# Kernel optimization log

Measured on AMD Instinct MI355X. Metric: run time of the kernel, lower is better.

Reference implementation:

```python
import jax, jax.numpy as jnp
import numpy as np

N, E = 50000, 800000
IN, HID, OUT, L = 512, 64, 40, 16
ALPHA, LAMBDA = 0.1, 0.5


def setup_inputs() -> dict:
    key = jax.random.key(0)
    ks = jax.random.split(key, 8)
    features = jax.random.normal(ks[0], (N, IN), jnp.float32)
    src = jax.random.randint(ks[1], (E,), 0, N)
    dst = jax.random.randint(ks[2], (E,), 0, N)
    # fcs[0]: Linear(IN, HID); fcs[1]: Linear(HID, OUT)
    W_in = jax.random.normal(ks[3], (IN, HID), jnp.float32) / np.sqrt(IN)
    b_in = jnp.zeros((HID,), jnp.float32)
    W_out = jax.random.normal(ks[4], (HID, OUT), jnp.float32) / np.sqrt(HID)
    b_out = jnp.zeros((OUT,), jnp.float32)
    # per-layer GCN2Conv weights (project_initial_features=False -> weight1 & weight2) + bias
    W1 = jax.random.normal(ks[5], (L, HID, HID), jnp.float32) / np.sqrt(HID)
    W2 = jax.random.normal(ks[6], (L, HID, HID), jnp.float32) / np.sqrt(HID)
    b = jnp.zeros((L, HID), jnp.float32)
    return dict(features=features, W_in=W_in, b_in=b_in, W1=W1, W2=W2, b=b,
                W_out=W_out, b_out=b_out, src=src, dst=dst)


def reference(features, W_in, b_in, W1, W2, b, W_out, b_out, src, dst):
    ones = jnp.ones((E,), jnp.float32)
    deg_out = jax.ops.segment_sum(ones, src, num_segments=N)
    deg_in = jax.ops.segment_sum(ones, dst, num_segments=N)
    norm_src = jnp.maximum(deg_out, 1.0) ** -0.5  # [N]
    norm_dst = jnp.maximum(deg_in, 1.0) ** -0.5   # [N]
    betas = jnp.log(LAMBDA / jnp.arange(1, L + 1, dtype=jnp.float32) + 1.0)

    # inference: dropout is identity
    h0 = jax.nn.relu(features @ W_in + b_in)  # [N, HID]

    def layer(h, params):
        w1, w2, bias, beta = params
        # symmetric-normalized sparse propagation: D^-1/2 A D^-1/2 h
        hs = h * norm_src[:, None]
        agg = jax.ops.segment_sum(hs[src], dst, num_segments=N) * norm_dst[:, None]
        f = (1.0 - ALPHA) * agg   # smoothed part
        f0 = ALPHA * h0           # initial residual
        rst = (1.0 - beta) * f + beta * (f @ w1)
        rst = rst + (1.0 - beta) * f0 + beta * (f0 @ w2)
        rst = rst + bias
        return jax.nn.relu(rst), None

    h, _ = jax.lax.scan(layer, h0, (W1, W2, b, betas))
    logits = h @ W_out + b_out  # [N, OUT]
    return jax.nn.log_softmax(logits, axis=1)
```

## Files before the change

### kernel.cpp

```cpp
#include <hip/hip_runtime.h>
#include <math.h>

#define NN 50000
#define NE 800000
#define INF 512
#define HID 64
#define OUTF 40
#define NL 16

#define NBLK 256
#define EPB 3125
#define NBUK 196
#define SLEN (NBUK * NBLK)

#define TN 32
#define FP 72

using short8 = __attribute__((ext_vector_type(8))) short;
using f32x4v = __attribute__((ext_vector_type(4))) float;

__device__ __forceinline__ unsigned int f2bf(float f) {
    unsigned int u = __float_as_uint(f);
    return (u + 0x7fffu + ((u >> 16) & 1u)) >> 16;
}
__device__ __forceinline__ float bflo(unsigned int w) { return __uint_as_float(w << 16); }
__device__ __forceinline__ float bfhi(unsigned int w) { return __uint_as_float(w & 0xffff0000u); }
__device__ __forceinline__ float bfs(unsigned short u) { return __uint_as_float(((unsigned)u) << 16); }


__global__ __launch_bounds__(256) void k_cnt(const int* __restrict__ src, const int* __restrict__ dst,
                                             int* __restrict__ cnt2) {
    __shared__ int hD[NBUK];
    __shared__ int hS[NBUK];
    int t = threadIdx.x;
    int blk = blockIdx.x;
    if (t < NBUK) { hD[t] = 0; hS[t] = 0; }
    __syncthreads();
    int s0 = blk * EPB;
    for (int i = t; i < EPB; i += 256) {
        int e = s0 + i;
        atomicAdd(&hD[dst[e] >> 8], 1);
        atomicAdd(&hS[src[e] >> 8], 1);
    }
    __syncthreads();
    if (t < NBUK) {
        cnt2[t * NBLK + blk] = hD[t];
        cnt2[SLEN + t * NBLK + blk] = hS[t];
    }
}

__global__ __launch_bounds__(256) void gscanA(const int* __restrict__ in, int* __restrict__ incl,
                                              int* __restrict__ bsum, int len) {
    __shared__ int lds[256];
    int i = blockIdx.x * 256 + threadIdx.x;
    int v = (i < len) ? in[i] : 0;
    lds[threadIdx.x] = v;
    __syncthreads();
    for (int off = 1; off < 256; off <<= 1) {
        int t = (threadIdx.x >= off) ? lds[threadIdx.x - off] : 0;
        __syncthreads();
        lds[threadIdx.x] += t;
        __syncthreads();
    }
    if (i < len) incl[i] = lds[threadIdx.x];
    if (threadIdx.x == 255) bsum[blockIdx.x] = lds[255];
}

__global__ __launch_bounds__(512) void gscanB(int* __restrict__ bsum, int nb) {
    __shared__ int lds[512];
    int v = (threadIdx.x < nb) ? bsum[threadIdx.x] : 0;
    lds[threadIdx.x] = v;
    __syncthreads();
    for (int off = 1; off < 512; off <<= 1) {
        int t = (threadIdx.x >= off) ? lds[threadIdx.x - off] : 0;
        __syncthreads();
        lds[threadIdx.x] += t;
        __syncthreads();
    }
    if (threadIdx.x < nb) bsum[threadIdx.x] = lds[threadIdx.x] - v;
}

__global__ __launch_bounds__(256) void gscanC(const int* __restrict__ incl, const int* __restrict__ in,
                                              const int* __restrict__ bsum, int* __restrict__ off, int len) {
    int i = blockIdx.x * 256 + threadIdx.x;
    if (i < len) off[i] = incl[i] - in[i] + bsum[i >> 8] - ((i >= SLEN) ? NE : 0);
}

__global__ __launch_bounds__(256) void k_scat(const int* __restrict__ src, const int* __restrict__ dst,
                                              const int* __restrict__ offD, const int* __restrict__ offS,
                                              uint2* __restrict__ edst, int* __restrict__ esrc) {
    __shared__ int cD[NBUK];
    __shared__ int cS[NBUK];
    int t = threadIdx.x;
    int blk = blockIdx.x;
    if (t < NBUK) { cD[t] = 0; cS[t] = 0; }
    __syncthreads();
    int s0 = blk * EPB;
    for (int i = t; i < EPB; i += 256) {
        int e = s0 + i;
        int d = dst[e];
        int s = src[e];
        int bD = d >> 8;
        int r = atomicAdd(&cD[bD], 1);
        uint2 v;
        v.x = (unsigned)d;
        v.y = (unsigned)s;
        edst[offD[bD * NBLK + blk] + r] = v;
        int bS = s >> 8;
        int r2 = atomicAdd(&cS[bS], 1);
        esrc[offS[bS * NBLK + blk] + r2] = s;
    }
}

__global__ __launch_bounds__(256) void k_build(const uint2* __restrict__ edst, const int* __restrict__ esrc,
                                               const int* __restrict__ offD, const int* __restrict__ offS,
                                               float* __restrict__ nd, int* __restrict__ row_start,
                                               int* __restrict__ col, float* __restrict__ ns) {
    __shared__ int cnt[256];
    __shared__ int ex[256];
    __shared__ int cur[256];
    int t = threadIdx.x;
    if (blockIdx.x < NBUK) {
        int b = blockIdx.x;
        int base = offD[b * NBLK];
        int end = (b < NBUK - 1) ? offD[(b + 1) * NBLK] : NE;
        cnt[t] = 0;
        __syncthreads();
        for (int p = base + t; p < end; p += 256) {
            uint2 ed = edst[p];
            atomicAdd(&cnt[ed.x & 255], 1);
        }
        __syncthreads();
        int v = cnt[t];
        ex[t] = v;
        __syncthreads();
        for (int off = 1; off < 256; off <<= 1) {
            int tv = (t >= off) ? ex[t - off] : 0;
            __syncthreads();
            ex[t] += tv;
            __syncthreads();
        }
        int excl = ex[t] - v;
        cur[t] = excl;
        int node = b * 256 + t;
        if (node < NN) {
            nd[node] = 1.0f / sqrtf((float)max(v, 1));
            row_start[node] = base + excl;
        }
        __syncthreads();
        for (int p = base + t; p < end; p += 256) {
            uint2 ed = edst[p];
            int r = atomicAdd(&cur[ed.x & 255], 1);
            col[base + r] = (int)ed.y;
        }
    } else {
        int b = blockIdx.x - NBUK;
        int base = offS[b * NBLK];
        int end = (b < NBUK - 1) ? offS[(b + 1) * NBLK] : NE;
        cnt[t] = 0;
        __syncthreads();
        for (int p = base + t; p < end; p += 256) {
            atomicAdd(&cnt[esrc[p] & 255], 1);
        }
        __syncthreads();
        int node = b * 256 + t;
        if (node < NN) ns[node] = 1.0f / sqrtf((float)max(cnt[t], 1));
    }
}

__global__ __launch_bounds__(256) void k_wpp(const float* __restrict__ W1, const float* __restrict__ W2,
                                             const float* __restrict__ Win,
                                             unsigned short* __restrict__ wc, unsigned short* __restrict__ wf) {
    int o = blockIdx.x * 256 + threadIdx.x;
    const int NWC = NL * 4 * 4 * 64 * 8;
    if (o < NWC) {
        int j = o & 7;
        int ln = (o >> 3) & 63;
        int c = (o >> 9) & 3;
        int s = (o >> 11) & 3;
        int l = o >> 13;
        int colg = c * 16 + (ln & 15);
        int k = (s & 1) * 32 + ((ln >> 4) << 3) + j;
        float beta = logf(0.5f / (float)(l + 1) + 1.0f);
        const float* W = (s < 2) ? W1 : W2;
        wc[o] = (unsigned short)f2bf(beta * W[((size_t)l * 64 + k) * 64 + colg]);
    } else if (o < NWC + 16 * 4 * 64 * 8) {
        int o2 = o - NWC;
        int jj = o2 & 7;
        int l = (o2 >> 3) & 63;
        int c = (o2 >> 9) & 3;
        int s = o2 >> 11;
        int colg = c * 16 + (l & 15);
        int k = s * 32 + ((l >> 4) << 3) + jj;
        wf[o2] = (unsigned short)f2bf(Win[k * HID + colg]);
    }
}

__global__ __launch_bounds__(256) void k_gemm0(const float* __restrict__ feat, const unsigned short* __restrict__ wf,
                                               float* __restrict__ p0, float* __restrict__ p1) {
    __shared__ unsigned int fS[2048];
    int tid = threadIdx.x;
    int lane = tid & 63;
    int wv = tid >> 6;
    int bx = blockIdx.x;
    int w = bx >> 1;
    int kh = bx & 1;
    int nb = w * 64;
    f32x4v acc[4];
#pragma unroll
    for (int c = 0; c < 4; c++) acc[c] = {0.0f, 0.0f, 0.0f, 0.0f};

    int k0 = kh * 256;
    for (int kc = k0; kc < k0 + 256; kc += 64) {
        if (kc != k0) __syncthreads();
        float4 t[4];
#pragma unroll
        for (int j = 0; j < 4; j++) {
            int i = tid + j * 256;
            int nl = i >> 4;
            int k4 = i & 15;
            int n = min(nb + nl, NN - 1);
            t[j] = *(const float4*)(feat + (size_t)n * INF + kc + k4 * 4);
        }
#pragma unroll
        for (int j = 0; j < 4; j++) {
            int i = tid + j * 256;
            int nl = i >> 4;
            int kl = (i & 15) * 4;
            int s = kl >> 5;
            int kk = kl & 31;
            int lslot = (nl & 15) | ((kk >> 3) << 4);
            int dstu = (((s * 4 + (nl >> 4)) * 64 + lslot) << 2) + ((kk & 4) >> 1);
            fS[dstu] = f2bf(t[j].x) | (f2bf(t[j].y) << 16);
            fS[dstu + 1] = f2bf(t[j].z) | (f2bf(t[j].w) << 16);
        }
        __syncthreads();
#pragma unroll
        for (int s = 0; s < 2; ++s) {
            int sg = (kc + s * 32) >> 5;
            short8 af = *(const short8*)&fS[((s * 4 + wv) * 64 + lane) << 2];
            short8 bf[4];
#pragma unroll
            for (int c = 0; c < 4; ++c)
                bf[c] = *(const short8*)(wf + ((size_t)(sg * 4 + c) * 64 + lane) * 8);
#pragma unroll
            for (int c = 0; c < 4; ++c)
                acc[c] = __builtin_amdgcn_mfma_f32_16x16x32_bf16(af, bf[c], acc[c], 0, 0, 0);
        }
    }
    float* p = kh ? p1 : p0;
    int nodeb = nb + (wv << 4) + ((lane >> 4) << 2);
    int colb = lane & 15;
#pragma unroll
    for (int r = 0; r < 4; ++r) {
        int node = nodeb + r;
        if (node < NN) {
            float* pp = p + (size_t)node * HID + colb;
#pragma unroll
            for (int c = 0; c < 4; ++c) pp[c * 16] = acc[c][r];
        }
    }
}

__global__ __launch_bounds__(256) void k_gfin(const float* __restrict__ p0, const float* __restrict__ p1,
                                              const float* __restrict__ bin, const float* __restrict__ ns,
                                              unsigned int* __restrict__ hs, unsigned int* __restrict__ f0b) {
    int i = blockIdx.x * 256 + threadIdx.x;
    if (i >= NN * 16) return;
    int node = i >> 4;
    int q = i & 15;
    float4 a = ((const float4*)p0)[i];
    float4 b = ((const float4*)p1)[i];
    float4 bi = ((const float4*)bin)[q];
    float nsv = ns[node];
    float q0 = fmaxf(a.x + b.x + bi.x, 0.0f);
    float q1 = fmaxf(a.y + b.y + bi.y, 0.0f);
    float q2 = fmaxf(a.z + b.z + bi.z, 0.0f);
    float q3 = fmaxf(a.w + b.w + bi.w, 0.0f);
    uint2 pk;
    pk.x = f2bf(q0 * nsv) | (f2bf(q1 * nsv) << 16);
    pk.y = f2bf(q2 * nsv) | (f2bf(q3 * nsv) << 16);
    *(uint2*)(hs + (size_t)node * 32 + q * 2) = pk;
    uint2 pf;
    pf.x = f2bf(q0 * 0.1f) | (f2bf(q1 * 0.1f) << 16);
    pf.y = f2bf(q2 * 0.1f) | (f2bf(q3 * 0.1f) << 16);
    *(uint2*)(f0b + (size_t)node * 32 + q * 2) = pf;
}

__global__ __launch_bounds__(256) void k_layer(const unsigned int* __restrict__ hs_in, const int* __restrict__ col,
                                               const int* __restrict__ row_start,
                                               const float* __restrict__ nd, const unsigned int* __restrict__ f0b,
                                               const unsigned short* __restrict__ wc, const float* __restrict__ bias,
                                               const float* __restrict__ ns, float omb,
                                               float* __restrict__ h, unsigned int* __restrict__ hs_out, int write_h) {
    __shared__ unsigned short fS[TN * FP];
    __shared__ unsigned short f0S[TN * FP];
    __shared__ unsigned short oS[TN * FP];
    __shared__ float nsS[TN];
    int tid = threadIdx.x;
    int lane = tid & 63;
    int wv = tid >> 6;
    int nb = blockIdx.x * TN;
    int g = lane >> 4;
    int ql = lane & 15;
    int half = ql >> 3;
    int qb = ql & 7;

    {
        int nl = tid >> 3, sg = tid & 7;
        int n = min(nb + nl, NN - 1);
        uint4 v = *(const uint4*)(f0b + (size_t)n * 32 + sg * 4);
        *(uint4*)&f0S[nl * FP + sg * 8] = v;
    }
    if (tid < TN) nsS[tid] = ns[min(nb + tid, NN - 1)];

    int nlP[2], baseP[2], degP[2], idxP[2];
    float ndP[2];
#pragma unroll
    for (int p = 0; p < 2; ++p) {
        int nl = p * 16 + wv * 4 + g;
        int n = min(nb + nl, NN - 1);
        nlP[p] = nl;
        int base = row_start[n];
        int nxt = (n < NN - 1) ? row_start[n + 1] : NE;
        baseP[p] = base;
        degP[p] = nxt - base;
        ndP[p] = nd[n];
    }
#pragma unroll
    for (int p = 0; p < 2; ++p) {
        idxP[p] = (ql < min(16, degP[p])) ? col[baseP[p] + ql] : 0;
    }

#pragma unroll
    for (int pass = 0; pass < 2; ++pass) {
        int base = baseP[pass];
        int deg = degP[pass];
        int idxv = idxP[pass];
        float a0 = 0.f, a1 = 0.f, a2 = 0.f, a3 = 0.f, a4 = 0.f, a5 = 0.f, a6 = 0.f, a7 = 0.f;
        for (int done = 0; done < deg; done += 16) {
            int cnt = min(16, deg - done);
            int nxt = done + 16;
            int idxn = 0;
            if (nxt < deg && ql < deg - nxt) idxn = col[base + nxt + ql];
            uint4 pv[4];
#pragma unroll
            for (int e = 0; e < 4; ++e) {
                int ec = 2 * e + half;
                int s = __shfl(idxv, (g << 4) | ec, 64);
                uint4 v = {0u, 0u, 0u, 0u};
                if (ec < cnt) v = *(const uint4*)(hs_in + (size_t)s * 32 + qb * 4);
                pv[e] = v;
            }
#pragma unroll
            for (int e = 0; e < 4; ++e) {
                a0 += bflo(pv[e].x); a1 += bfhi(pv[e].x);
                a2 += bflo(pv[e].y); a3 += bfhi(pv[e].y);
                a4 += bflo(pv[e].z); a5 += bfhi(pv[e].z);
                a6 += bflo(pv[e].w); a7 += bfhi(pv[e].w);
            }
#pragma unroll
            for (int e = 0; e < 4; ++e) {
                int ec = 8 + 2 * e + half;
                int s = __shfl(idxv, (g << 4) | ec, 64);
                uint4 v = {0u, 0u, 0u, 0u};
                if (ec < cnt) v = *(const uint4*)(hs_in + (size_t)s * 32 + qb * 4);
                pv[e] = v;
            }
#pragma unroll
            for (int e = 0; e < 4; ++e) {
                a0 += bflo(pv[e].x); a1 += bfhi(pv[e].x);
                a2 += bflo(pv[e].y); a3 += bfhi(pv[e].y);
                a4 += bflo(pv[e].z); a5 += bfhi(pv[e].z);
                a6 += bflo(pv[e].w); a7 += bfhi(pv[e].w);
            }
            idxv = idxn;
        }
        a0 += __shfl_xor(a0, 8, 64);
        a1 += __shfl_xor(a1, 8, 64);
        a2 += __shfl_xor(a2, 8, 64);
        a3 += __shfl_xor(a3, 8, 64);
        a4 += __shfl_xor(a4, 8, 64);
        a5 += __shfl_xor(a5, 8, 64);
        a6 += __shfl_xor(a6, 8, 64);
        a7 += __shfl_xor(a7, 8, 64);
        float sc = 0.9f * ndP[pass];
        int nl = nlP[pass];
        if (half == 0) {
            uint4 w;
            w.x = f2bf(a0 * sc) | (f2bf(a1 * sc) << 16);
            w.y = f2bf(a2 * sc) | (f2bf(a3 * sc) << 16);
            w.z = f2bf(a4 * sc) | (f2bf(a5 * sc) << 16);
            w.w = f2bf(a6 * sc) | (f2bf(a7 * sc) << 16);
            *(uint4*)&fS[nl * FP + qb * 8] = w;
        }
    }
    __syncthreads();

    int hi = lane >> 4;
    int lo = lane & 15;
    f32x4v acc0 = {0.0f, 0.0f, 0.0f, 0.0f};
    f32x4v acc1 = {0.0f, 0.0f, 0.0f, 0.0f};
#pragma unroll
    for (int s = 0; s < 4; ++s) {
        short8 bf = *(const short8*)(wc + ((size_t)(s * 4 + wv) * 64 + lane) * 8);
        const unsigned short* ab = (s < 2) ? fS : f0S;
        int ko = (s & 1) * 32;
        short8 a0 = *(const short8*)&ab[(0 * 16 + lo) * FP + ko + hi * 8];
        short8 a1 = *(const short8*)&ab[(1 * 16 + lo) * FP + ko + hi * 8];
        acc0 = __builtin_amdgcn_mfma_f32_16x16x32_bf16(a0, bf, acc0, 0, 0, 0);
        acc1 = __builtin_amdgcn_mfma_f32_16x16x32_bf16(a1, bf, acc1, 0, 0, 0);
    }

    int colg = wv * 16 + lo;
    float bv = bias[colg];
#pragma unroll
    for (int m = 0; m < 2; ++m) {
        f32x4v a = m ? acc1 : acc0;
#pragma unroll
        for (int r = 0; r < 4; ++r) {
            int rowl = m * 16 + hi * 4 + r;
            float fv = bfs(fS[rowl * FP + colg]);
            float f0v = bfs(f0S[rowl * FP + colg]);
            float q = fmaxf(a[r] + omb * (fv + f0v) + bv, 0.0f);
            oS[rowl * FP + colg] = (unsigned short)f2bf(q * nsS[rowl]);
            if (write_h) {
                int node = nb + rowl;
                if (node < NN) h[(size_t)node * HID + colg] = q;
            }
        }
    }
    __syncthreads();

    {
        int nl = tid >> 3, sg = tid & 7;
        int node = nb + nl;
        if (node < NN) {
            uint4 v = *(const uint4*)&oS[nl * FP + sg * 8];
            *(uint4*)(hs_out + (size_t)node * 32 + sg * 4) = v;
        }
    }
}

__global__ __launch_bounds__(256) void k_out(const float* __restrict__ h, const float* __restrict__ Wout,
                                             const float* __restrict__ bout, float* __restrict__ out) {
    __shared__ float red_mx[4][64];
    __shared__ float red_s[4][64];
    int tid = threadIdx.x;
    int lane = tid & 63;
    int wv = tid >> 6;
    int half = wv & 1;
    int grp = wv >> 1;
    int node = blockIdx.x * 128 + grp * 64 + lane;
    int nodec = min(node, NN - 1);
    float acc[20];
#pragma unroll
    for (int c = 0; c < 20; c++) acc[c] = 0.0f;
    const float4* hr = (const float4*)(h + (size_t)nodec * HID);
    const float* wb = Wout + half * 20;
    for (int kk = 0; kk < HID / 4; ++kk) {
        float4 a = hr[kk];
        float av[4] = {a.x, a.y, a.z, a.w};
#pragma unroll
        for (int j = 0; j < 4; j++) {
            const float* wr = wb + (size_t)(kk * 4 + j) * OUTF;
#pragma unroll
            for (int c = 0; c < 20; c++) acc[c] += av[j] * wr[c];
        }
    }
    const float* bp = bout + half * 20;
#pragma unroll
    for (int c = 0; c < 20; c++) acc[c] += bp[c];
    float mx = acc[0];
#pragma unroll
    for (int c = 1; c < 20; c++) mx = fmaxf(mx, acc[c]);
    red_mx[wv][lane] = mx;
    __syncthreads();
    float gmx = fmaxf(mx, red_mx[wv ^ 1][lane]);
    float s = 0.0f;
#pragma unroll
    for (int c = 0; c < 20; c++) s += expf(acc[c] - gmx);
    red_s[wv][lane] = s;
    __syncthreads();
    float lse = logf(s + red_s[wv ^ 1][lane]) + gmx;
    if (node < NN) {
        float4* op = (float4*)(out + (size_t)node * OUTF + half * 20);
#pragma unroll
        for (int q = 0; q < 5; q++) {
            float4 v;
            v.x = acc[q * 4 + 0] - lse;
            v.y = acc[q * 4 + 1] - lse;
            v.z = acc[q * 4 + 2] - lse;
            v.w = acc[q * 4 + 3] - lse;
            op[q] = v;
        }
    }
}

extern "C" void kernel_launch(void* const* d_in, const int* in_sizes, int n_in,
                              void* d_out, int out_size, void* d_ws, size_t ws_size,
                              hipStream_t stream) {
    const float* feat = (const float*)d_in[0];
    const float* Win  = (const float*)d_in[1];
    const float* bin  = (const float*)d_in[2];
    const float* W1   = (const float*)d_in[3];
    const float* W2   = (const float*)d_in[4];
    const float* bvec = (const float*)d_in[5];
    const float* Wout = (const float*)d_in[6];
    const float* bout = (const float*)d_in[7];
    const int*   src  = (const int*)d_in[8];
    const int*   dst  = (const int*)d_in[9];
    float* out = (float*)d_out;

    char* ws = (char*)d_ws;
    size_t off = 0;
    auto take = [&](size_t bytes) {
        void* p = ws + off;
        off += (bytes + 255) & ~(size_t)255;
        return p;
    };
    int* bsum      = (int*)take(512 * 4);
    int* row_start = (int*)take(NN * 4);
    int* col       = (int*)take(NE * 4);
    float* nsrc    = (float*)take(NN * 4);
    float* ndst    = (float*)take(NN * 4);
    int* cnt2      = (int*)take(2 * SLEN * 4);
    int* off2      = (int*)take(2 * SLEN * 4);
    int* sincl     = (int*)take(2 * SLEN * 4);
    unsigned short* wcat  = (unsigned short*)take((size_t)NL * 4 * 4 * 64 * 8 * 2);
    unsigned short* wfrag = (unsigned short*)take((size_t)INF * HID * 2);
    unsigned int* f0b = (unsigned int*)take((size_t)NN * HID * 2);
    float* hbuf    = (float*)take((size_t)NN * HID * 4);
    float* part1   = (float*)take((size_t)NN * HID * 4);
    unsigned int* hsA = (unsigned int*)take((size_t)NN * HID * 2);
    unsigned int* hsB = (unsigned int*)take((size_t)NN * HID * 2);

    uint2* edst = (uint2*)hbuf;
    int* esrc   = (int*)part1;
    int* offD = off2;
    int* offS = off2 + SLEN;

    const int NB_W = (NN + 63) / 64;
    const int NB_L = (NN + TN - 1) / TN;
    const int NB_O = (NN + 127) / 128;
    const int NB_S2 = 2 * SLEN / 256;

    k_cnt<<<NBLK, 256, 0, stream>>>(src, dst, cnt2);
    gscanA<<<NB_S2, 256, 0, stream>>>(cnt2, sincl, bsum, 2 * SLEN);
    gscanB<<<1, 512, 0, stream>>>(bsum, NB_S2);
    gscanC<<<NB_S2, 256, 0, stream>>>(sincl, cnt2, bsum, off2, 2 * SLEN);
    k_scat<<<NBLK, 256, 0, stream>>>(src, dst, offD, offS, edst, esrc);
    k_build<<<2 * NBUK, 256, 0, stream>>>(edst, esrc, offD, offS, ndst, row_start, col, nsrc);

    k_wpp<<<(NL * 4 * 4 * 64 * 8 + INF * HID + 255) / 256, 256, 0, stream>>>(W1, W2, Win, wcat, wfrag);
    k_gemm0<<<2 * NB_W, 256, 0, stream>>>(feat, wfrag, hbuf, part1);
    k_gfin<<<(NN * 16 + 255) / 256, 256, 0, stream>>>(hbuf, part1, bin, nsrc, hsA, f0b);

    for (int l = 0; l < NL; ++l) {
        const unsigned int* hin = (l & 1) ? hsB : hsA;
        unsigned int* hout = (l & 1) ? hsA : hsB;
        float beta = logf(0.5f / (float)(l + 1) + 1.0f);
        float omb = 1.0f - beta;
        k_layer<<<NB_L, 256, 0, stream>>>(hin, col, row_start, ndst, f0b,
                                          wcat + (size_t)l * 4 * 4 * 64 * 8, bvec + l * HID,
                                          nsrc, omb, hbuf, hout, (l == NL - 1) ? 1 : 0);
    }
    k_out<<<NB_O, 256, 0, stream>>>(hbuf, Wout, bout, out);
}
```

Measured before the change: 557.5 us.

## Balance layer aggregation across edges with packed dst ids and LDS atomic accumulation

```diff
diff --git a/kernel.cpp b/kernel.cpp
--- a/kernel.cpp
+++ b/kernel.cpp
@@ -15,6 +15,7 @@
 
 #define TN 32
 #define FP 72
+#define TNP 33
 
 using short8 = __attribute__((ext_vector_type(8))) short;
 using f32x4v = __attribute__((ext_vector_type(4))) float;
@@ -115,7 +116,7 @@
 __global__ __launch_bounds__(256) void k_build(const uint2* __restrict__ edst, const int* __restrict__ esrc,
                                                const int* __restrict__ offD, const int* __restrict__ offS,
                                                float* __restrict__ nd, int* __restrict__ row_start,
-                                               int* __restrict__ col, float* __restrict__ ns) {
+                                               int* __restrict__ epk, float* __restrict__ ns) {
     __shared__ int cnt[256];
     __shared__ int ex[256];
     __shared__ int cur[256];
@@ -151,7 +152,7 @@
         for (int p = base + t; p < end; p += 256) {
             uint2 ed = edst[p];
             int r = atomicAdd(&cur[ed.x & 255], 1);
-            col[base + r] = (int)ed.y;
+            epk[base + r] = (int)((ed.y << 5) | (ed.x & 31u));
         }
     } else {
         int b = blockIdx.x - NBUK;
@@ -287,16 +288,18 @@
     *(uint2*)(f0b + (size_t)node * 32 + q * 2) = pf;
 }
 
-__global__ __launch_bounds__(256) void k_layer(const unsigned int* __restrict__ hs_in, const int* __restrict__ col,
+__global__ __launch_bounds__(256) void k_layer(const unsigned int* __restrict__ hs_in, const int* __restrict__ epk,
                                                const int* __restrict__ row_start,
                                                const float* __restrict__ nd, const unsigned int* __restrict__ f0b,
                                                const unsigned short* __restrict__ wc, const float* __restrict__ bias,
                                                const float* __restrict__ ns, float omb,
                                                float* __restrict__ h, unsigned int* __restrict__ hs_out, int write_h) {
+    __shared__ float fT32[HID * TNP];
     __shared__ unsigned short fS[TN * FP];
     __shared__ unsigned short f0S[TN * FP];
     __shared__ unsigned short oS[TN * FP];
     __shared__ float nsS[TN];
+    __shared__ float ndS[TN];
     int tid = threadIdx.x;
     int lane = tid & 63;
     int wv = tid >> 6;
@@ -306,94 +309,98 @@
     int half = ql >> 3;
     int qb = ql & 7;
 
+    for (int i = tid; i < HID * TNP; i += 256) fT32[i] = 0.0f;
     {
         int nl = tid >> 3, sg = tid & 7;
         int n = min(nb + nl, NN - 1);
         uint4 v = *(const uint4*)(f0b + (size_t)n * 32 + sg * 4);
         *(uint4*)&f0S[nl * FP + sg * 8] = v;
     }
-    if (tid < TN) nsS[tid] = ns[min(nb + tid, NN - 1)];
-
-    int nlP[2], baseP[2], degP[2], idxP[2];
-    float ndP[2];
-#pragma unroll
-    for (int p = 0; p < 2; ++p) {
-        int nl = p * 16 + wv * 4 + g;
-        int n = min(nb + nl, NN - 1);
-        nlP[p] = nl;
-        int base = row_start[n];
-        int nxt = (n < NN - 1) ? row_start[n + 1] : NE;
-        baseP[p] = base;
-        degP[p] = nxt - base;
-        ndP[p] = nd[n];
-    }
-#pragma unroll
-    for (int p = 0; p < 2; ++p) {
-        idxP[p] = (ql < min(16, degP[p])) ? col[baseP[p] + ql] : 0;
-    }
-
-#pragma unroll
-    for (int pass = 0; pass < 2; ++pass) {
-        int base = baseP[pass];
-        int deg = degP[pass];
-        int idxv = idxP[pass];
+    if (tid < TN) {
+        nsS[tid] = ns[min(nb + tid, NN - 1)];
+        ndS[tid] = nd[min(nb + tid, NN - 1)];
+    }
+    int base = row_start[nb];
+    int end = (nb + TN < NN) ? row_start[nb + TN] : NE;
+    __syncthreads();
+
+    {
+        int gid = wv * 4 + g;
+        int E = end - base;
+        int len = (E + 15) >> 4;
+        int g0 = base + gid * len;
+        int g1 = min(g0 + len, end);
         float a0 = 0.f, a1 = 0.f, a2 = 0.f, a3 = 0.f, a4 = 0.f, a5 = 0.f, a6 = 0.f, a7 = 0.f;
-        for (int done = 0; done < deg; done += 16) {
-            int cnt = min(16, deg - done);
-            int nxt = done + 16;
+        int cur = -1;
+        int idxv = 0;
+        if (g0 < g1) {
+            int c0 = min(16, g1 - g0);
+            idxv = (ql < c0) ? epk[g0 + ql] : 0;
+        }
+#define FLUSHRUN()                                                          \
+        do {                                                                \
+            float* fd = &fT32[(qb * 8) * TNP + cur];                        \
+            atomicAdd(fd + 0 * TNP, a0);                                    \
+            atomicAdd(fd + 1 * TNP, a1);                                    \
+            atomicAdd(fd + 2 * TNP, a2);                                    \
+            atomicAdd(fd + 3 * TNP, a3);                                    \
+            atomicAdd(fd + 4 * TNP, a4);                                    \
+            atomicAdd(fd + 5 * TNP, a5);                                    \
+            atomicAdd(fd + 6 * TNP, a6);                                    \
+            atomicAdd(fd + 7 * TNP, a7);                                    \
+            a0 = a1 = a2 = a3 = a4 = a5 = a6 = a7 = 0.f;                    \
+        } while (0)
+        for (int c = g0; c < g1; c += 16) {
+            int cnt = min(16, g1 - c);
+            int nxtc = c + 16;
             int idxn = 0;
-            if (nxt < deg && ql < deg - nxt) idxn = col[base + nxt + ql];
+            if (nxtc < g1 && ql < g1 - nxtc) idxn = epk[nxtc + ql];
+            unsigned ue[4];
             uint4 pv[4];
-#pragma unroll
-            for (int e = 0; e < 4; ++e) {
-                int ec = 2 * e + half;
-                int s = __shfl(idxv, (g << 4) | ec, 64);
-                uint4 v = {0u, 0u, 0u, 0u};
-                if (ec < cnt) v = *(const uint4*)(hs_in + (size_t)s * 32 + qb * 4);
-                pv[e] = v;
+#define GATHER4(OFF)                                                        \
+            _Pragma("unroll")                                               \
+            for (int e = 0; e < 4; ++e) {                                   \
+                int ec = (OFF) + 2 * e + half;                              \
+                unsigned u = (unsigned)__shfl(idxv, (g << 4) | ec, 64);     \
+                ue[e] = u;                                                  \
+                uint4 v = {0u, 0u, 0u, 0u};                                 \
+                if (ec < cnt) v = *(const uint4*)(hs_in + (size_t)(u >> 5) * 32 + qb * 4); \
+                pv[e] = v;                                                  \
             }
-#pragma unroll
-            for (int e = 0; e < 4; ++e) {
-                a0 += bflo(pv[e].x); a1 += bfhi(pv[e].x);
-                a2 += bflo(pv[e].y); a3 += bfhi(pv[e].y);
-                a4 += bflo(pv[e].z); a5 += bfhi(pv[e].z);
-                a6 += bflo(pv[e].w); a7 += bfhi(pv[e].w);
+#define ACCUM4(OFF)                                                         \
+            _Pragma("unroll")                                               \
+            for (int e = 0; e < 4; ++e) {                                   \
+                int ec = (OFF) + 2 * e + half;                              \
+                if (ec < cnt) {                                             \
+                    int dl = (int)(ue[e] & 31u);                            \
+                    if (dl != cur) {                                        \
+                        if (cur >= 0) FLUSHRUN();                           \
+                        cur = dl;                                           \
+                    }                                                       \
+                    a0 += bflo(pv[e].x); a1 += bfhi(pv[e].x);               \
+                    a2 += bflo(pv[e].y); a3 += bfhi(pv[e].y);               \
+                    a4 += bflo(pv[e].z); a5 += bfhi(pv[e].z);               \
+                    a6 += bflo(pv[e].w); a7 += bfhi(pv[e].w);               \
+                }                                                           \
             }
-#pragma unroll
-            for (int e = 0; e < 4; ++e) {
-                int ec = 8 + 2 * e + half;
-                int s = __shfl(idxv, (g << 4) | ec, 64);
-                uint4 v = {0u, 0u, 0u, 0u};
-                if (ec < cnt) v = *(const uint4*)(hs_in + (size_t)s * 32 + qb * 4);
-                pv[e] = v;
-            }
-#pragma unroll
-            for (int e = 0; e < 4; ++e) {
-                a0 += bflo(pv[e].x); a1 += bfhi(pv[e].x);
-                a2 += bflo(pv[e].y); a3 += bfhi(pv[e].y);
-                a4 += bflo(pv[e].z); a5 += bfhi(pv[e].z);
-                a6 += bflo(pv[e].w); a7 += bfhi(pv[e].w);
-            }
+            GATHER4(0)
+            ACCUM4(0)
+            GATHER4(8)
+            ACCUM4(8)
+#undef GATHER4
+#undef ACCUM4
             idxv = idxn;
         }
-        a0 += __shfl_xor(a0, 8, 64);
-        a1 += __shfl_xor(a1, 8, 64);
-        a2 += __shfl_xor(a2, 8, 64);
-        a3 += __shfl_xor(a3, 8, 64);
-        a4 += __shfl_xor(a4, 8, 64);
-        a5 += __shfl_xor(a5, 8, 64);
-        a6 += __shfl_xor(a6, 8, 64);
-        a7 += __shfl_xor(a7, 8, 64);
-        float sc = 0.9f * ndP[pass];
-        int nl = nlP[pass];
-        if (half == 0) {
-            uint4 w;
-            w.x = f2bf(a0 * sc) | (f2bf(a1 * sc) << 16);
-            w.y = f2bf(a2 * sc) | (f2bf(a3 * sc) << 16);
-            w.z = f2bf(a4 * sc) | (f2bf(a5 * sc) << 16);
-            w.w = f2bf(a6 * sc) | (f2bf(a7 * sc) << 16);
-            *(uint4*)&fS[nl * FP + qb * 8] = w;
-        }
+        if (cur >= 0) FLUSHRUN();
+#undef FLUSHRUN
+    }
+    __syncthreads();
+
+    for (int i = tid; i < HID * TN; i += 256) {
+        int d = i >> 5;
+        int nl = i & 31;
+        float v = fT32[d * TNP + nl] * (0.9f * ndS[nl]);
+        fS[nl * FP + d] = (unsigned short)f2bf(v);
     }
     __syncthreads();
 
@@ -521,7 +528,7 @@
     };
     int* bsum      = (int*)take(512 * 4);
     int* row_start = (int*)take(NN * 4);
-    int* col       = (int*)take(NE * 4);
+    int* epk       = (int*)take(NE * 4);
     float* nsrc    = (float*)take(NN * 4);
     float* ndst    = (float*)take(NN * 4);
     int* cnt2      = (int*)take(2 * SLEN * 4);
@@ -550,7 +557,7 @@
     gscanB<<<1, 512, 0, stream>>>(bsum, NB_S2);
     gscanC<<<NB_S2, 256, 0, stream>>>(sincl, cnt2, bsum, off2, 2 * SLEN);
     k_scat<<<NBLK, 256, 0, stream>>>(src, dst, offD, offS, edst, esrc);
-    k_build<<<2 * NBUK, 256, 0, stream>>>(edst, esrc, offD, offS, ndst, row_start, col, nsrc);
+    k_build<<<2 * NBUK, 256, 0, stream>>>(edst, esrc, offD, offS, ndst, row_start, epk, nsrc);
 
     k_wpp<<<(NL * 4 * 4 * 64 * 8 + INF * HID + 255) / 256, 256, 0, stream>>>(W1, W2, Win, wcat, wfrag);
     k_gemm0<<<2 * NB_W, 256, 0, stream>>>(feat, wfrag, hbuf, part1);
@@ -561,7 +568,7 @@
         unsigned int* hout = (l & 1) ? hsA : hsB;
         float beta = logf(0.5f / (float)(l + 1) + 1.0f);
         float omb = 1.0f - beta;
-        k_layer<<<NB_L, 256, 0, stream>>>(hin, col, row_start, ndst, f0b,
+        k_layer<<<NB_L, 256, 0, stream>>>(hin, epk, row_start, ndst, f0b,
                                           wcat + (size_t)l * 4 * 4 * 64 * 8, bvec + l * HID,
                                           nsrc, omb, hbuf, hout, (l == NL - 1) ? 1 : 0);
     }
```

New measurement: 1.249 ms. +124.0%, slower.
